# Kernel tuning notes

Hardware: AMD Instinct MI355X
Metric: run time of the kernel (lower is better)

The kernel has to match this reference:

```python
import jax, jax.numpy as jnp
import numpy as np

K = 9          # kernel_size (number of KNN neighbours), dilation=1
SCALAR = 20.0  # scalar in _build_explain
EPS = 1e-10


def setup_inputs() -> dict:
    key = jax.random.key(0)
    ks = jax.random.split(key, 9)
    B, C, H, W = 16, 192, 28, 28
    Cout, r = 384, 16
    f = lambda k, s, sc: jax.random.normal(k, s, jnp.float32) * sc
    return {
        "x": f(ks[0], (B, C, H, W), 1.0),
        "w_edge": f(ks[1], (Cout, 2 * C), 0.05),  # 1x1 conv on concat[x_i, x_j-x_i]
        "b_edge": f(ks[2], (Cout,), 0.05),
        "w1": f(ks[3], (C // r, C), 0.1),          # CBAM channel MLP (shared)
        "b1": f(ks[4], (C // r,), 0.1),
        "w2": f(ks[5], (C, C // r), 0.1),
        "b2": f(ks[6], (C,), 0.1),
        "w_sp": f(ks[7], (1, 2, 7, 7), 0.1),       # CBAM spatial 7x7 conv
        "b_sp": f(ks[8], (1,), 0.1),
    }


def _cbam(x, w1, b1, w2, b2, w_sp, b_sp):
    # Standard CBAM: channel gate (avg+max pooled -> shared MLP -> sigmoid)
    # then spatial gate (channel mean/max -> 7x7 conv -> sigmoid).
    mlp = lambda v: jax.nn.relu(v @ w1.T + b1) @ w2.T + b2
    ch = jax.nn.sigmoid(mlp(x.mean((2, 3))) + mlp(x.max((2, 3))))
    x = x * ch[:, :, None, None]
    sp_in = jnp.stack([x.mean(1), x.max(1)], axis=1)  # (B,2,H,W)
    sp = jax.lax.conv_general_dilated(sp_in, w_sp, (1, 1), [(3, 3), (3, 3)])
    return x * jax.nn.sigmoid(sp + b_sp[None, :, None, None])


def _build_explain(att_x):
    B, C, H, W = att_x.shape
    a = jax.nn.softmax(att_x.reshape(B, C, H * W), axis=2)
    a = a / (a.max(axis=2, keepdims=True) + EPS)
    return (2.0 * a - 1.0) / (2.0 * SCALAR) + 1.0  # (B,C,N)


def _knn_idx(xf):
    # DenseDilatedKnnGraph: L2-normalize over channels, pairwise sq-dist, topk.
    xn = xf / jnp.maximum(jnp.linalg.norm(xf, axis=1, keepdims=True), 1e-12)
    xt = jnp.swapaxes(xn, 1, 2)                      # (B,N,C)
    sq = jnp.sum(xt * xt, axis=-1)                   # (B,N)
    dist = sq[:, :, None] - 2.0 * jnp.einsum("bnc,bmc->bnm", xt, xt) + sq[:, None, :]
    _, idx = jax.lax.top_k(-dist, K)                 # nn_idx = edge_index[0], (B,N,K)
    return idx


def reference(x, w_edge, b_edge, w1, b1, w2, b2, w_sp, b_sp):
    B, C, H, W = x.shape
    N = H * W
    xf = x.reshape(B, C, N)
    idx = _knn_idx(xf)                               # dynamic KNN graph (B,N,K)
    att = _build_explain(_cbam(x, w1, b1, w2, b2, w_sp, b_sp))
    xf = xf * att
    # EdgeConv2d: x_i = center (edge_index[1] is arange -> broadcast),
    # x_j gathered by neighbour indices.
    x_i = xf[:, :, :, None]                           # (B,C,N,1)
    x_e = jnp.broadcast_to(x_i, (B, C, N, K))
    i_e = jnp.broadcast_to(idx[:, None, :, :], (B, C, N, K))
    x_j = jnp.take_along_axis(x_e, i_e, axis=2)       # (B,C,N,K)
    feat = jnp.concatenate([x_e, x_j - x_i], axis=1)  # (B,2C,N,K)
    out = jnp.einsum("oc,bcnk->bonk", w_edge, feat) + b_edge[None, :, None, None]
    out = jax.nn.relu(out)                            # BasicConv: 1x1 conv + relu
    out = out.max(axis=-1)                            # max over neighbours (B,O,N)
    return out.reshape(B, -1, H, W)
```

## Files before the change

### kernel.cpp

```cpp
#include <hip/hip_runtime.h>
#include <math.h>

#define HW 784
#define Cc 192
#define Bb 16
#define CO 384
#define KK 9
#define OG 8

typedef __attribute__((ext_vector_type(8))) short bf16x8;
typedef __attribute__((ext_vector_type(4))) float f32x4;

__device__ __forceinline__ unsigned f2ord(float f){
  unsigned u = __float_as_uint(f);
  return (u & 0x80000000u) ? ~u : (u | 0x80000000u);
}

__device__ __forceinline__ unsigned short b16rne(float v){
  unsigned u = __float_as_uint(v);
  unsigned r = u + 0x7FFFu + ((u >> 16) & 1u);
  return (unsigned short)(r >> 16);
}

__global__ void k_chstats(const float* __restrict__ x, float* __restrict__ chm, float* __restrict__ chx){
  int wid = threadIdx.x >> 6, lane = threadIdx.x & 63;
  int r = blockIdx.x * 4 + wid;
  const float4* row = (const float4*)(x + (size_t)r * HW);
  float s = 0.f, m = -3.4e38f;
  #pragma unroll
  for (int i = 0; i < 4; ++i){
    int f4 = lane + 64*i;
    if (f4 < 196){
      float4 v = row[f4];
      s += v.x + v.y + v.z + v.w;
      m = fmaxf(m, fmaxf(fmaxf(v.x, v.y), fmaxf(v.z, v.w)));
    }
  }
  for (int off = 32; off; off >>= 1){ s += __shfl_xor(s, off); m = fmaxf(m, __shfl_xor(m, off)); }
  if (lane == 0){ chm[r] = s / (float)HW; chx[r] = m; }
}

__global__ void k_mlp(const float* __restrict__ chm, const float* __restrict__ chx,
                      const float* __restrict__ w1, const float* __restrict__ b1,
                      const float* __restrict__ w2, const float* __restrict__ b2,
                      float* __restrict__ chv){
  int b = blockIdx.x, t = threadIdx.x;
  __shared__ float vm[Cc], vx[Cc], hp[2][12];
  if (t < Cc){ vm[t] = chm[b*Cc + t]; vx[t] = chx[b*Cc + t]; }
  __syncthreads();
  if (t < 24){
    int h = t % 12;
    const float* src = (t < 12) ? vm : vx;
    float a = b1[h];
    for (int c = 0; c < Cc; ++c) a += src[c] * w1[h*Cc + c];
    hp[t/12][h] = fmaxf(a, 0.f);
  }
  __syncthreads();
  if (t < Cc){
    float a = 2.f * b2[t];
    for (int h = 0; h < 12; ++h) a += (hp[0][h] + hp[1][h]) * w2[t*12 + h];
    chv[b*Cc + t] = 1.f / (1.f + expf(-a));
  }
}

__global__ void k_spin(const float* __restrict__ x, const float* __restrict__ chv,
                       float* __restrict__ amean, float* __restrict__ amax,
                       float* __restrict__ nrm){
  int b = blockIdx.x >> 2;
  int n = ((blockIdx.x & 3) << 8) + threadIdx.x;
  if (n >= HW) return;
  const float* xb = x + (size_t)b*Cc*HW + n;
  const float* cb = chv + b*Cc;
  float s = 0.f, m = -3.4e38f, sq = 0.f;
  for (int c = 0; c < Cc; ++c){
    float xv = xb[(size_t)c*HW];
    float v = xv * cb[c];
    s += v; m = fmaxf(m, v); sq += xv*xv;
  }
  amean[b*HW + n] = s / (float)Cc;
  amax[b*HW + n]  = m;
  nrm[b*HW + n]   = fmaxf(sqrtf(sq), 1e-12f);
}

__global__ void k_conv(const float* __restrict__ amean, const float* __restrict__ amax,
                       const float* __restrict__ wsp, const float* __restrict__ bsp,
                       float* __restrict__ satt){
  int b = blockIdx.x >> 2;
  int n = ((blockIdx.x & 3) << 8) + threadIdx.x;
  if (n >= HW) return;
  int yy = n / 28, xx = n % 28;
  float a = 0.f;
  for (int ky = 0; ky < 7; ++ky){
    int iy = yy + ky - 3; if (iy < 0 || iy >= 28) continue;
    for (int kx = 0; kx < 7; ++kx){
      int ix = xx + kx - 3; if (ix < 0 || ix >= 28) continue;
      int ii = b*HW + iy*28 + ix;
      a += amean[ii]*wsp[ky*7 + kx] + amax[ii]*wsp[49 + ky*7 + kx];
    }
  }
  satt[b*HW + n] = 1.f / (1.f + expf(-(a + bsp[0])));
}

__global__ void k_attstats(const float* __restrict__ x, const float* __restrict__ chv,
                           const float* __restrict__ satt,
                           float* __restrict__ vmaxA, float* __restrict__ invA){
  int wid = threadIdx.x >> 6, lane = threadIdx.x & 63;
  int r = blockIdx.x * 4 + wid;
  int b = r / Cc;
  const float4* row = (const float4*)(x + (size_t)r * HW);
  const float4* sr  = (const float4*)(satt + b * HW);
  float ch = chv[r];
  float4 vv[4];
  float m = -3.4e38f;
  #pragma unroll
  for (int i = 0; i < 4; ++i){
    int f4 = lane + 64*i;
    if (f4 < 196){
      float4 xv = row[f4], sv = sr[f4];
      vv[i].x = (xv.x * ch) * sv.x; vv[i].y = (xv.y * ch) * sv.y;
      vv[i].z = (xv.z * ch) * sv.z; vv[i].w = (xv.w * ch) * sv.w;
      m = fmaxf(m, fmaxf(fmaxf(vv[i].x, vv[i].y), fmaxf(vv[i].z, vv[i].w)));
    }
  }
  for (int off = 32; off; off >>= 1) m = fmaxf(m, __shfl_xor(m, off));
  float s = 0.f;
  #pragma unroll
  for (int i = 0; i < 4; ++i){
    int f4 = lane + 64*i;
    if (f4 < 196){
      s += expf(vv[i].x - m) + expf(vv[i].y - m) + expf(vv[i].z - m) + expf(vv[i].w - m);
    }
  }
  for (int off = 32; off; off >>= 1) s += __shfl_xor(s, off);
  if (lane == 0){ vmaxA[r] = m; invA[r] = 1.f / (1.f + 1e-10f * s); }
}

__global__ __launch_bounds__(256) void k_cvt2wp(const float* __restrict__ x, const float* __restrict__ nrm,
                                                const float* __restrict__ chv, const float* __restrict__ satt,
                                                const float* __restrict__ vmaxA, const float* __restrict__ invA,
                                                const float* __restrict__ we,
                                                unsigned short* __restrict__ Xnh, unsigned short* __restrict__ Xnl,
                                                unsigned short* __restrict__ XAh, unsigned short* __restrict__ XAl,
                                                unsigned short* __restrict__ Wph, unsigned short* __restrict__ Wpl){
  int bid = blockIdx.x, t = threadIdx.x;
  if (bid >= 624){
    int i = (bid - 624)*256 + t;
    int o = i / Cc, c = i % Cc;
    float v = (o < CO) ? (we[(size_t)o*384 + c] - we[(size_t)o*384 + Cc + c])
                       : we[(size_t)(o - CO)*384 + Cc + c];
    unsigned short h = b16rne(v);
    float lo = v - __uint_as_float((unsigned)h << 16);
    Wph[i] = h;
    Wpl[i] = b16rne(lo);
    return;
  }
  int xx = bid % 13, yy = (bid / 13) % 3, b = bid / 39;
  int c0 = yy*64, n0 = xx*64;
  __shared__ float T[64][65];
  __shared__ float chs[64], vms[64], ivs[64];
  int nl = (t & 15) * 4, cl = t >> 4;
  const float* xb = x + (size_t)b*Cc*HW;
  #pragma unroll
  for (int r = 0; r < 4; ++r){
    int c_loc = cl + r*16;
    int n = n0 + nl;
    float4 v = (n < HW) ? *(const float4*)(xb + (size_t)(c0 + c_loc)*HW + n) : make_float4(0,0,0,0);
    *(float4*)&T[c_loc][nl] = v;
  }
  if (t < 64){
    chs[t] = chv[b*Cc + c0 + t];
    vms[t] = vmaxA[b*Cc + c0 + t];
    ivs[t] = invA[b*Cc + c0 + t];
  }
  __syncthreads();
  int nr = t >> 2, q = t & 3;
  int n_g = n0 + nr;
  if (n_g >= HW) return;
  float nv = nrm[b*HW + n_g];
  float sr = satt[b*HW + n_g];
  unsigned int nh[8], nlw[8], ah[8], al[8];
  #pragma unroll
  for (int j = 0; j < 8; ++j){
    unsigned int parts[2][2];
    #pragma unroll
    for (int e = 0; e < 2; ++e){
      int cc_ = q*16 + 2*j + e;
      float v = T[cc_][nr];
      float xnv = v / nv;
      unsigned short h0 = b16rne(xnv);
      float l0 = xnv - __uint_as_float((unsigned)h0 << 16);
      parts[0][e] = (unsigned)h0 | ((unsigned)b16rne(l0) << 16);
      float vvv = (v * chs[cc_]) * sr;
      float ex = expf(vvv - vms[cc_]);
      float a = ex * ivs[cc_];
      float xav = v * ((2.f*a - 1.f)*0.025f + 1.f);
      unsigned short h1 = b16rne(xav);
      float l1 = xav - __uint_as_float((unsigned)h1 << 16);
      parts[1][e] = (unsigned)h1 | ((unsigned)b16rne(l1) << 16);
    }
    nh[j]  = (parts[0][0] & 0xFFFFu) | (parts[0][1] << 16);
    nlw[j] = (parts[0][0] >> 16)     | (parts[0][1] & 0xFFFF0000u);
    ah[j]  = (parts[1][0] & 0xFFFFu) | (parts[1][1] << 16);
    al[j]  = (parts[1][0] >> 16)     | (parts[1][1] & 0xFFFF0000u);
  }
  size_t base = ((size_t)b*HW + n_g)*Cc + c0 + q*16;
  *(uint4*)(Xnh + base)     = make_uint4(nh[0], nh[1], nh[2], nh[3]);
  *(uint4*)(Xnh + base + 8) = make_uint4(nh[4], nh[5], nh[6], nh[7]);
  *(uint4*)(Xnl + base)     = make_uint4(nlw[0], nlw[1], nlw[2], nlw[3]);
  *(uint4*)(Xnl + base + 8) = make_uint4(nlw[4], nlw[5], nlw[6], nlw[7]);
  *(uint4*)(XAh + base)     = make_uint4(ah[0], ah[1], ah[2], ah[3]);
  *(uint4*)(XAh + base + 8) = make_uint4(ah[4], ah[5], ah[6], ah[7]);
  *(uint4*)(XAl + base)     = make_uint4(al[0], al[1], al[2], al[3]);
  *(uint4*)(XAl + base + 8) = make_uint4(al[4], al[5], al[6], al[7]);
}

__global__ __launch_bounds__(256) void k_gramgemm(const unsigned short* __restrict__ Xnh,
                                                  const unsigned short* __restrict__ Xnl,
                                                  const unsigned short* __restrict__ Wph,
                                                  const unsigned short* __restrict__ Wpl,
                                                  const unsigned short* __restrict__ XAh,
                                                  const unsigned short* __restrict__ XAl,
                                                  float* __restrict__ D, float* __restrict__ PQ){
  __shared__ __align__(16) char smem[32768];
  unsigned short* Als = (unsigned short*)smem;
  unsigned short* Bls = Als + 8192;
  float* Tt = (float*)smem;

  int hwbid = blockIdx.x;
  int bid = (hwbid & 7) * 140 + (hwbid >> 3);
  int t = threadIdx.x, w = t >> 6, l = t & 63;
  int wr = w >> 1, wc = w & 1;
  f32x4 acc[4][4] = {};
  int nn = t >> 1, half = t & 1;

  bool isGram = bid < 448;
  int b, r0, c0, ty = 0, tx = 0;
  const unsigned short *A_h, *A_l, *B_h, *B_l;
  if (isGram){
    b = bid / 28; int rm = bid % 28;
    if      (rm <  7){ ty=0; tx=rm; }
    else if (rm < 13){ ty=1; tx=1+rm-7; }
    else if (rm < 18){ ty=2; tx=2+rm-13; }
    else if (rm < 22){ ty=3; tx=3+rm-18; }
    else if (rm < 25){ ty=4; tx=4+rm-22; }
    else if (rm < 27){ ty=5; tx=5+rm-25; }
    else             { ty=6; tx=6; }
    r0 = ty*128; c0 = tx*128;
    size_t bb = (size_t)b*HW*Cc;
    A_h = Xnh + bb; A_l = Xnl + bb; B_h = Xnh + bb; B_l = Xnl + bb;
  } else {
    int id = bid - 448;
    b = id / 42; int rem = id % 42;
    c0 = (rem % 7) * 128; r0 = (rem / 7) * 128;
    size_t bb = (size_t)b*HW*Cc;
    A_h = Wph; A_l = Wpl; B_h = XAh + bb; B_l = XAl + bb;
  }
  int ra = r0 + nn; if (isGram && ra > HW-1) ra = HW-1;
  int rb = c0 + nn; if (rb > HW-1) rb = HW-1;

  for (int cc = 0; cc < 9; ++cc){
    int seg = cc/3, kc0 = (cc%3)*64;
    const unsigned short* As_ = (seg < 2 ? A_h : A_l);
    const unsigned short* Bs_ = (seg == 1 ? B_l : B_h);
    const uint4* ga = (const uint4*)(As_ + (size_t)ra*Cc + kc0 + half*32);
    const uint4* gb = (const uint4*)(Bs_ + (size_t)rb*Cc + kc0 + half*32);
    uint4 va0 = ga[0], va1 = ga[1], va2 = ga[2], va3 = ga[3];
    uint4 vb0 = gb[0], vb1 = gb[1], vb2 = gb[2], vb3 = gb[3];
    __syncthreads();
    int base = nn*128 + half*64;
    int sw = (nn & 7) << 4;
    *(uint4*)((char*)Als + ((base      ) ^ sw)) = va0;
    *(uint4*)((char*)Als + ((base + 16 ) ^ sw)) = va1;
    *(uint4*)((char*)Als + ((base + 32 ) ^ sw)) = va2;
    *(uint4*)((char*)Als + ((base + 48 ) ^ sw)) = va3;
    *(uint4*)((char*)Bls + ((base      ) ^ sw)) = vb0;
    *(uint4*)((char*)Bls + ((base + 16 ) ^ sw)) = vb1;
    *(uint4*)((char*)Bls + ((base + 32 ) ^ sw)) = vb2;
    *(uint4*)((char*)Bls + ((base + 48 ) ^ sw)) = vb3;
    __syncthreads();
    #pragma unroll
    for (int ks = 0; ks < 2; ++ks){
      bf16x8 af[4], bfr[4];
      int kb = ks*64 + (l >> 4)*16;
      #pragma unroll
      for (int mt = 0; mt < 4; ++mt){
        int rl = wr*64 + mt*16 + (l & 15);
        int off = (rl*128 + kb) ^ ((rl & 7) << 4);
        af[mt] = *(const bf16x8*)((const char*)Als + off);
      }
      #pragma unroll
      for (int nt = 0; nt < 4; ++nt){
        int cl2 = wc*64 + nt*16 + (l & 15);
        int off = (cl2*128 + kb) ^ ((cl2 & 7) << 4);
        bfr[nt] = *(const bf16x8*)((const char*)Bls + off);
      }
      #pragma unroll
      for (int mt = 0; mt < 4; ++mt)
        #pragma unroll
        for (int nt = 0; nt < 4; ++nt)
          acc[mt][nt] = __builtin_amdgcn_mfma_f32_16x16x32_bf16(af[mt], bfr[nt], acc[mt][nt], 0, 0, 0);
    }
  }
  if (isGram){
    #pragma unroll
    for (int mt = 0; mt < 4; ++mt){
      #pragma unroll
      for (int nt = 0; nt < 4; ++nt){
        int col = c0 + wc*64 + nt*16 + (l & 15);
        if (col >= HW) continue;
        int row0 = r0 + wr*64 + mt*16 + ((l >> 4) << 2);
        #pragma unroll
        for (int r = 0; r < 4; ++r){
          int row = row0 + r;
          if (row < HW) D[((size_t)b*HW + row)*HW + col] = -acc[mt][nt][r];
        }
      }
    }
    if (tx > ty){
      #pragma unroll
      for (int nt = 0; nt < 4; ++nt){
        __syncthreads();
        int ci = wc*16 + (l & 15);
        #pragma unroll
        for (int mt = 0; mt < 4; ++mt){
          int row = wr*64 + mt*16 + ((l >> 4) << 2);
          #pragma unroll
          for (int r = 0; r < 4; ++r)
            Tt[ci*129 + row + r] = -acc[mt][nt][r];
        }
        __syncthreads();
        int ci2 = t >> 3;
        int col = c0 + (ci2 >> 4)*64 + nt*16 + (ci2 & 15);
        if (col < HW){
          float* Drow = D + ((size_t)b*HW + col)*HW + r0;
          int rbase = (t & 7)*16;
          #pragma unroll
          for (int j = 0; j < 4; ++j){
            int rr = rbase + j*4;
            float4 v = make_float4(Tt[ci2*129 + rr],     Tt[ci2*129 + rr + 1],
                                   Tt[ci2*129 + rr + 2], Tt[ci2*129 + rr + 3]);
            *(float4*)(Drow + rr) = v;
          }
        }
      }
    }
  } else {
    #pragma unroll
    for (int mt = 0; mt < 4; ++mt){
      #pragma unroll
      for (int nt = 0; nt < 4; ++nt){
        int col = c0 + wc*64 + nt*16 + (l & 15);
        if (col >= HW) continue;
        int row0 = r0 + wr*64 + mt*16 + ((l >> 4) << 2);
        #pragma unroll
        for (int r = 0; r < 4; ++r){
          PQ[((size_t)b*768 + row0 + r)*HW + col] = acc[mt][nt][r];
        }
      }
    }
  }
}

__global__ __launch_bounds__(256) void k_select(const float* __restrict__ D, int* __restrict__ idxo){
  int wid = threadIdx.x >> 6, lane = threadIdx.x & 63;
  int row = blockIdx.x * 4 + wid;
  const float* Dr = D + (size_t)row * HW;
  float dvv[13]; int mvv[13];
  #pragma unroll
  for (int i = 0; i < 13; ++i){
    int m = lane + 64*i;
    dvv[i] = (m < HW) ? Dr[m] : 3.4e38f;
    mvv[i] = m;
  }
  for (int k = 0; k < KK; ++k){
    float bd = dvv[0]; int bi = 0;
    #pragma unroll
    for (int i = 1; i < 13; ++i) if (dvv[i] < bd){ bd = dvv[i]; bi = i; }
    unsigned long long key = ((unsigned long long)f2ord(bd) << 32) | (unsigned)mvv[bi];
    for (int off = 32; off; off >>= 1){
      unsigned long long o = __shfl_xor(key, off);
      if (o < key) key = o;
    }
    int wm = (int)(unsigned)(key & 0xffffffffu);
    if (lane == 0) idxo[(size_t)k*(Bb*HW) + row] = wm;
    if (mvv[bi] == wm) dvv[bi] = 3.4e38f;
  }
}

__global__ __launch_bounds__(256) void k_edge(const float* __restrict__ PQ, const int* __restrict__ idx,
                                              const float* __restrict__ be, float* __restrict__ out){
  int bid = blockIdx.x;
  int b = bid / (CO/OG), og = bid % (CO/OG);
  int o0 = og * OG;
  __shared__ float Qls[OG][HW + 4];
  const float* Qbase = PQ + ((size_t)b*768 + CO + o0)*HW;
  int t = threadIdx.x;
  #pragma unroll
  for (int oo = 0; oo < OG; ++oo){
    if (t < 196) *(float4*)&Qls[oo][t*4] = *(const float4*)(Qbase + (size_t)oo*HW + t*4);
  }
  __syncthreads();
  const float* Pbase = PQ + ((size_t)b*768 + o0)*HW;
  float bev[OG];
  #pragma unroll
  for (int oo = 0; oo < OG; ++oo) bev[oo] = be[o0 + oo];
  for (int n = t; n < HW; n += 256){
    int ip[KK];
    #pragma unroll
    for (int k = 0; k < KK; ++k) ip[k] = idx[(size_t)k*(Bb*HW) + b*HW + n];
    float qm[OG];
    #pragma unroll
    for (int oo = 0; oo < OG; ++oo) qm[oo] = -3.4e38f;
    #pragma unroll
    for (int k = 0; k < KK; ++k){
      int j = ip[k];
      #pragma unroll
      for (int oo = 0; oo < OG; ++oo) qm[oo] = fmaxf(qm[oo], Qls[oo][j]);
    }
    #pragma unroll
    for (int oo = 0; oo < OG; ++oo){
      out[((size_t)b*CO + o0 + oo)*HW + n] = fmaxf(Pbase[(size_t)oo*HW + n] + bev[oo] + qm[oo], 0.f);
    }
  }
}

extern "C" void kernel_launch(void* const* d_in, const int* in_sizes, int n_in,
                              void* d_out, int out_size, void* d_ws, size_t ws_size,
                              hipStream_t stream){
  const float* x   = (const float*)d_in[0];
  const float* we  = (const float*)d_in[1];
  const float* be  = (const float*)d_in[2];
  const float* w1  = (const float*)d_in[3];
  const float* b1  = (const float*)d_in[4];
  const float* w2  = (const float*)d_in[5];
  const float* b2  = (const float*)d_in[6];
  const float* wsp = (const float*)d_in[7];
  const float* bsp = (const float*)d_in[8];
  float* out = (float*)d_out;

  float* ws    = (float*)d_ws;
  float* chm   = ws;
  float* chx   = chm + 3072;
  float* chv   = chx + 3072;
  float* vmaxA = chv + 3072;
  float* invA  = vmaxA + 3072;
  float* amean = invA + 3072;
  float* amax  = amean + 12544;
  float* satt  = amax + 12544;
  float* nrm   = satt + 12544;
  unsigned short* Wph = (unsigned short*)(nrm + 12544);
  unsigned short* Wpl = Wph + 147456;
  unsigned short* Xnh = Wpl + 147456;
  unsigned short* Xnl = Xnh + 2408448;
  unsigned short* XAh = Xnl + 2408448;
  unsigned short* XAl = XAh + 2408448;
  int*   idx   = (int*)(XAl + 2408448);
  float* D     = (float*)(idx + 112896);
  float* PQ    = D + 9834496;

  k_chstats<<<768, 256, 0, stream>>>(x, chm, chx);
  k_mlp<<<16, 192, 0, stream>>>(chm, chx, w1, b1, w2, b2, chv);
  k_spin<<<64, 256, 0, stream>>>(x, chv, amean, amax, nrm);
  k_conv<<<64, 256, 0, stream>>>(amean, amax, wsp, bsp, satt);
  k_attstats<<<768, 256, 0, stream>>>(x, chv, satt, vmaxA, invA);
  k_cvt2wp<<<1200, 256, 0, stream>>>(x, nrm, chv, satt, vmaxA, invA, we,
                                     Xnh, Xnl, XAh, XAl, Wph, Wpl);
  k_gramgemm<<<1120, 256, 0, stream>>>(Xnh, Xnl, Wph, Wpl, XAh, XAl, D, PQ);
  k_select<<<3136, 256, 0, stream>>>(D, idx);
  k_edge<<<Bb*(CO/OG), 256, 0, stream>>>(PQ, idx, be, out);
}
```

Baseline: 142.6 us.

## Load MFMA fragments directly from global memory and vectorize select loads

The gram/projection GEMM no longer stages A and B tiles through swizzled shared memory with two barriers per chunk. Each lane instead loads its bf16x8 MFMA fragments straight from global memory, relying on L1/L2 for reuse across waves. Shared memory is cut down to the transpose scratch buffer. The select kernel now reads distance rows with float4 loads plus a scalar tail. This removes LDS traffic and synchronisation, at the risk of redundant global loads and poorer coalescing, since each 16-byte row segment is fetched by multiple waves.

```diff
diff --git a/kernel.cpp b/kernel.cpp
--- a/kernel.cpp
+++ b/kernel.cpp
@@ -221,17 +221,13 @@
                                                   const unsigned short* __restrict__ XAh,
                                                   const unsigned short* __restrict__ XAl,
                                                   float* __restrict__ D, float* __restrict__ PQ){
-  __shared__ __align__(16) char smem[32768];
-  unsigned short* Als = (unsigned short*)smem;
-  unsigned short* Bls = Als + 8192;
-  float* Tt = (float*)smem;
+  __shared__ float Tt[32*129];
 
   int hwbid = blockIdx.x;
   int bid = (hwbid & 7) * 140 + (hwbid >> 3);
   int t = threadIdx.x, w = t >> 6, l = t & 63;
   int wr = w >> 1, wc = w & 1;
   f32x4 acc[4][4] = {};
-  int nn = t >> 1, half = t & 1;
 
   bool isGram = bid < 448;
   int b, r0, c0, ty = 0, tx = 0;
@@ -255,45 +251,31 @@
     size_t bb = (size_t)b*HW*Cc;
     A_h = Wph; A_l = Wpl; B_h = XAh + bb; B_l = XAl + bb;
   }
-  int ra = r0 + nn; if (isGram && ra > HW-1) ra = HW-1;
-  int rb = c0 + nn; if (rb > HW-1) rb = HW-1;
+
+  int rowA[4], rowB[4];
+  #pragma unroll
+  for (int mt = 0; mt < 4; ++mt){
+    int r = r0 + wr*64 + mt*16 + (l & 15);
+    if (isGram && r > HW-1) r = HW-1;
+    rowA[mt] = r * Cc;
+    int c = c0 + wc*64 + mt*16 + (l & 15);
+    if (c > HW-1) c = HW-1;
+    rowB[mt] = c * Cc;
+  }
+  int ko_lane = (l >> 4) * 8;
 
   for (int cc = 0; cc < 9; ++cc){
     int seg = cc/3, kc0 = (cc%3)*64;
     const unsigned short* As_ = (seg < 2 ? A_h : A_l);
     const unsigned short* Bs_ = (seg == 1 ? B_l : B_h);
-    const uint4* ga = (const uint4*)(As_ + (size_t)ra*Cc + kc0 + half*32);
-    const uint4* gb = (const uint4*)(Bs_ + (size_t)rb*Cc + kc0 + half*32);
-    uint4 va0 = ga[0], va1 = ga[1], va2 = ga[2], va3 = ga[3];
-    uint4 vb0 = gb[0], vb1 = gb[1], vb2 = gb[2], vb3 = gb[3];
-    __syncthreads();
-    int base = nn*128 + half*64;
-    int sw = (nn & 7) << 4;
-    *(uint4*)((char*)Als + ((base      ) ^ sw)) = va0;
-    *(uint4*)((char*)Als + ((base + 16 ) ^ sw)) = va1;
-    *(uint4*)((char*)Als + ((base + 32 ) ^ sw)) = va2;
-    *(uint4*)((char*)Als + ((base + 48 ) ^ sw)) = va3;
-    *(uint4*)((char*)Bls + ((base      ) ^ sw)) = vb0;
-    *(uint4*)((char*)Bls + ((base + 16 ) ^ sw)) = vb1;
-    *(uint4*)((char*)Bls + ((base + 32 ) ^ sw)) = vb2;
-    *(uint4*)((char*)Bls + ((base + 48 ) ^ sw)) = vb3;
-    __syncthreads();
     #pragma unroll
     for (int ks = 0; ks < 2; ++ks){
+      int ko = kc0 + ks*32 + ko_lane;
       bf16x8 af[4], bfr[4];
-      int kb = ks*64 + (l >> 4)*16;
-      #pragma unroll
-      for (int mt = 0; mt < 4; ++mt){
-        int rl = wr*64 + mt*16 + (l & 15);
-        int off = (rl*128 + kb) ^ ((rl & 7) << 4);
-        af[mt] = *(const bf16x8*)((const char*)Als + off);
-      }
-      #pragma unroll
-      for (int nt = 0; nt < 4; ++nt){
-        int cl2 = wc*64 + nt*16 + (l & 15);
-        int off = (cl2*128 + kb) ^ ((cl2 & 7) << 4);
-        bfr[nt] = *(const bf16x8*)((const char*)Bls + off);
-      }
+      #pragma unroll
+      for (int mt = 0; mt < 4; ++mt) af[mt] = *(const bf16x8*)(As_ + rowA[mt] + ko);
+      #pragma unroll
+      for (int nt = 0; nt < 4; ++nt) bfr[nt] = *(const bf16x8*)(Bs_ + rowB[nt] + ko);
       #pragma unroll
       for (int mt = 0; mt < 4; ++mt)
         #pragma unroll
@@ -301,6 +283,7 @@
           acc[mt][nt] = __builtin_amdgcn_mfma_f32_16x16x32_bf16(af[mt], bfr[nt], acc[mt][nt], 0, 0, 0);
     }
   }
+
   if (isGram){
     #pragma unroll
     for (int mt = 0; mt < 4; ++mt){
@@ -365,12 +348,21 @@
   int wid = threadIdx.x >> 6, lane = threadIdx.x & 63;
   int row = blockIdx.x * 4 + wid;
   const float* Dr = D + (size_t)row * HW;
+  const float4* Dr4 = (const float4*)Dr;
   float dvv[13]; int mvv[13];
   #pragma unroll
-  for (int i = 0; i < 13; ++i){
-    int m = lane + 64*i;
-    dvv[i] = (m < HW) ? Dr[m] : 3.4e38f;
-    mvv[i] = m;
+  for (int j = 0; j < 3; ++j){
+    float4 v = Dr4[lane + 64*j];
+    int m0 = 4*(lane + 64*j);
+    dvv[j*4+0] = v.x; mvv[j*4+0] = m0;
+    dvv[j*4+1] = v.y; mvv[j*4+1] = m0+1;
+    dvv[j*4+2] = v.z; mvv[j*4+2] = m0+2;
+    dvv[j*4+3] = v.w; mvv[j*4+3] = m0+3;
+  }
+  {
+    int m = 768 + lane;
+    dvv[12] = (m < HW) ? Dr[m] : 3.4e38f;
+    mvv[12] = m;
   }
   for (int k = 0; k < KK; ++k){
     float bd = dvv[0]; int bi = 0;
```

Measured after the change: 186.6 us. 30.8% more time.
